# Optimization experiments

Hardware: AMD Instinct MI355X
Metric: run time of the kernel (lower is better)

## Reference

```python
import jax, jax.numpy as jnp
import numpy as np

N, n, D1, D2 = 16, 1024, 64, 64


def setup_inputs() -> dict:
    key = jax.random.key(0)
    ks = jax.random.split(key, 17)
    f = lambda k, shape: jax.random.normal(k, shape, dtype=jnp.float32)
    return {
        "A": f(ks[0], (N, n, n)),
        "X": f(ks[1], (N, n, D1)),
        "coeffs": f(ks[2], (5,)),
        "wA1": f(ks[3], (1, D1)),
        "wA2": f(ks[4], (1, D1)),
        "w11": f(ks[5], (D2, D1)),
        "w12": f(ks[6], (D2, D1)),
        "w13": f(ks[7], (D2, 1)),
        "w14": f(ks[8], (D2, 1)),
        "w15": f(ks[9], (D2, 1)),
        "w16": f(ks[10], (D2, 1)),
        "w21": f(ks[11], (D2, D1)),
        "w22": f(ks[12], (D2, D1)),
        "w23": f(ks[13], (D2, 1)),
        "w24": f(ks[14], (D2, 1)),
        "w25": f(ks[15], (D2, 1)),
        "w26": f(ks[16], (D2, 1)),
    }


def reference(A, X, coeffs, wA1, wA2, w11, w12, w13, w14, w15, w16,
              w21, w22, w23, w24, w25, w26):
    nn_ = A.shape[-1]
    diag = jnp.diagonal(A, axis1=-2, axis2=-1)          # (N, n)
    mean_diag = diag.mean(-1)                            # (N,)
    rowmean = A.mean(-1)                                 # (N, n) mean over columns
    mean_all = rowmean.mean(-1)                          # (N,)
    mean_X = X.mean(1)                                   # (N, D1)

    p1 = X @ wA1[0]                                      # (N, n)   Linear(D1->1) per node
    p2 = mean_X @ wA2[0]                                 # (N,)     Linear(D1->1) on mean

    # adjacency transform: scalar-weighted A + scalar stats + symmetrized row stats
    A_t = (coeffs[0] * A
           + (coeffs[1] * mean_all + coeffs[2] * mean_diag + p2)[:, None, None]
           + coeffs[3] * (rowmean[:, None, :] + rowmean[:, :, None])
           + coeffs[4] * (diag[:, None, :] + diag[:, :, None])
           + p1[:, None, :] + p1[:, :, None])             # (N, n, n)

    def node_transform(w_x, w_mx, w_col, w_diag, w_mdiag, w_mall):
        per_graph = (mean_X @ w_mx.T                      # (N, D2)
                     + mean_diag[:, None] * w_mdiag[:, 0][None, :]
                     + mean_all[:, None] * w_mall[:, 0][None, :])
        return (jnp.einsum('bnd,ed->bne', X, w_x)         # (N, n, D2)
                + rowmean[:, :, None] * w_col[:, 0]
                + diag[:, :, None] * w_diag[:, 0]
                + per_graph[:, None, :])

    X1_t = node_transform(w11, w12, w13, w14, w15, w16)
    X2_t = node_transform(w21, w22, w23, w24, w25, w26)

    out = A_t @ X2_t / nn_ + X1_t                         # (N, n, D2)
    return (A_t, out)
```

## Files before the change

### kernel.cpp

```cpp
#include <hip/hip_runtime.h>
#include <hip/hip_bf16.h>

#define NGRAPH 16
#define NNODE 1024
#define DDIM 64

typedef __attribute__((ext_vector_type(8))) short bf16x8;
typedef __attribute__((ext_vector_type(4))) float f32x4;

#define OFF_ROWSUM 0
#define OFF_DIAG   16384
#define OFF_P1     32768
#define OFF_R      49152
#define OFF_CS     65536
#define OFF_S      73728
#define OFF_S2P    75840
#define OFF_R2P    92224
#define OFF_BASE0  110656
#define OFF_X2T    1159232

__device__ __forceinline__ unsigned short f2bf(float f) {
    unsigned int u = __float_as_uint(f);
    u = (u + 0x7fffu + ((u >> 16) & 1u)) >> 16;
    return (unsigned short)u;
}

__device__ __forceinline__ float wave_reduce(float v) {
    #pragma unroll
    for (int off = 32; off; off >>= 1) v += __shfl_down(v, off, 64);
    return v;
}

__global__ __launch_bounds__(256) void kA_stats(const float* __restrict__ A,
                                                const float* __restrict__ X,
                                                const float* __restrict__ wA1,
                                                float* __restrict__ rowsum,
                                                float* __restrict__ diagv,
                                                float* __restrict__ p1,
                                                float* __restrict__ colsum_part) {
    if (blockIdx.x < NGRAPH * NNODE / 4) {
        int row  = blockIdx.x * 4 + (threadIdx.x >> 6);
        int lane = threadIdx.x & 63;
        const float4* b4 = (const float4*)(A + (size_t)row * NNODE);
        float sum = 0.f;
        #pragma unroll
        for (int it = 0; it < 4; ++it) {
            float4 v = b4[lane + it * 64];
            sum += v.x + v.y + v.z + v.w;
        }
        sum = wave_reduce(sum);
        if (lane == 0) {
            rowsum[row] = sum;
            int i = row & (NNODE - 1);
            diagv[row] = ((const float*)b4)[i];
        }
    } else {
        int bid  = blockIdx.x - NGRAPH * NNODE / 4;
        int b    = bid >> 3;
        int blk  = bid & 7;
        int wv   = threadIdx.x >> 6;
        int lane = threadIdx.x & 63;
        float w = wA1[lane];
        float cs = 0.f;
        int row0 = blk * 128 + wv * 32;
        const float* Xb = X + (size_t)b * NNODE * DDIM;
        for (int rI = 0; rI < 32; ++rI) {
            int i = row0 + rI;
            float x = Xb[i * DDIM + lane];
            cs += x;
            float v = wave_reduce(x * w);
            if (lane == 0) p1[b * NNODE + i] = v;
        }
        __shared__ float csl[4][64];
        csl[wv][lane] = cs;
        __syncthreads();
        if (threadIdx.x < 64) {
            float t = csl[0][lane] + csl[1][lane] + csl[2][lane] + csl[3][lane];
            colsum_part[(b * 8 + blk) * 64 + lane] = t;
        }
    }
}

__global__ __launch_bounds__(256) void kB_nodes(const float* __restrict__ X,
                                                const float* __restrict__ coeffs,
                                                const float* __restrict__ wA2,
                                                const float* __restrict__ w11,
                                                const float* __restrict__ w12,
                                                const float* __restrict__ w13,
                                                const float* __restrict__ w14,
                                                const float* __restrict__ w15,
                                                const float* __restrict__ w16,
                                                const float* __restrict__ w21,
                                                const float* __restrict__ w22,
                                                const float* __restrict__ w23,
                                                const float* __restrict__ w24,
                                                const float* __restrict__ w25,
                                                const float* __restrict__ w26,
                                                const float* __restrict__ rowsum,
                                                const float* __restrict__ diagv,
                                                const float* __restrict__ colsum_part,
                                                const float* __restrict__ p1g,
                                                float* __restrict__ rws,
                                                float* __restrict__ base0,
                                                unsigned short* __restrict__ x2tg,
                                                float* __restrict__ S2part,
                                                float* __restrict__ R2part,
                                                float* __restrict__ sArr) {
    __shared__ float Xl[64][68];
    __shared__ float w1l[64][68];
    __shared__ float w2l[64][68];
    __shared__ unsigned short X2Tl[64][68];
    __shared__ float rm_l[64], dg_l[64], r_l[64];
    __shared__ float redS[4][64], redR[4][64];
    __shared__ float redA[4], redD[4];
    __shared__ float mxs[64], p2s;
    __shared__ float pg1_l[64], pg2_l[64];

    int b    = blockIdx.x >> 4;
    int tile = blockIdx.x & 15;
    int i0   = tile * 64;
    int tid  = threadIdx.x;
    int e    = tid & 63;
    int wv   = tid >> 6;

    const float* Xg = X + (size_t)b * (NNODE * DDIM) + (size_t)i0 * DDIM;
    #pragma unroll
    for (int it = 0; it < 4; ++it) {
        int g   = it * 256 + tid;
        int row = g >> 4;
        int c4  = (g & 15) << 2;
        float4 v  = ((const float4*)Xg)[g];
        *(float4*)&Xl[row][c4] = v;
        float4 v1 = ((const float4*)w11)[g];
        *(float4*)&w1l[row][c4] = v1;
        float4 v2 = ((const float4*)w21)[g];
        *(float4*)&w2l[row][c4] = v2;
    }

    float sa = 0.f, sd = 0.f;
    for (int i = tid; i < NNODE; i += 256) {
        sa += rowsum[b * NNODE + i];
        sd += diagv[b * NNODE + i];
    }
    sa = wave_reduce(sa); sd = wave_reduce(sd);
    if (e == 0) { redA[wv] = sa; redD[wv] = sd; }
    if (tid < 64) {
        float mx = 0.f;
        for (int k = 0; k < 8; ++k) mx += colsum_part[(b * 8 + k) * 64 + tid];
        mxs[tid] = mx * (1.f / (float)NNODE);
    }
    __syncthreads();
    float mean_all  = (redA[0] + redA[1] + redA[2] + redA[3]) * (1.f / ((float)NNODE * (float)NNODE));
    float mean_diag = (redD[0] + redD[1] + redD[2] + redD[3]) * (1.f / (float)NNODE);
    if (tid < 64) {
        float v = wave_reduce(mxs[tid] * wA2[tid]);
        if (tid == 0) p2s = v;
    }
    if (tid < 64) {
        float a1 = 0.f, a2 = 0.f;
        for (int d = 0; d < 64; ++d) {
            float m = mxs[d];
            a1 += m * w12[tid * 64 + d];
            a2 += m * w22[tid * 64 + d];
        }
        pg1_l[tid] = a1 + mean_diag * w15[tid] + mean_all * w16[tid];
        pg2_l[tid] = a2 + mean_diag * w25[tid] + mean_all * w26[tid];
    }
    float c3 = coeffs[3], c4c = coeffs[4];
    if (tid < 64) {
        float rs  = rowsum[b * NNODE + i0 + tid];
        float dgv = diagv[b * NNODE + i0 + tid];
        float rmv = rs * (1.f / (float)NNODE);
        rm_l[tid] = rmv;
        dg_l[tid] = dgv;
        float rv = c3 * rmv + c4c * dgv + p1g[b * NNODE + i0 + tid];
        r_l[tid] = rv;
        rws[b * NNODE + i0 + tid] = rv;
    }
    __syncthreads();
    if (tile == 0 && tid == 0)
        sArr[b] = coeffs[1] * mean_all + coeffs[2] * mean_diag + p2s;

    float w13e = w13[e], w14e = w14[e], w23e = w23[e], w24e = w24[e];
    float pg1e = pg1_l[e], pg2e = pg2_l[e];

    float acc1[16], acc2[16];
    #pragma unroll
    for (int t = 0; t < 16; ++t) { acc1[t] = 0.f; acc2[t] = 0.f; }

    for (int d0 = 0; d0 < 64; d0 += 4) {
        float4 w1v = *(const float4*)&w1l[e][d0];
        float4 w2v = *(const float4*)&w2l[e][d0];
        #pragma unroll
        for (int t = 0; t < 16; ++t) {
            int li = wv + 4 * t;
            float4 xv = *(const float4*)&Xl[li][d0];
            acc1[t] += xv.x * w1v.x + xv.y * w1v.y + xv.z * w1v.z + xv.w * w1v.w;
            acc2[t] += xv.x * w2v.x + xv.y * w2v.y + xv.z * w2v.z + xv.w * w2v.w;
        }
    }

    float s2acc = 0.f, r2acc = 0.f;
    #pragma unroll
    for (int t = 0; t < 16; ++t) {
        int li = wv + 4 * t;
        int i  = i0 + li;
        float rmv = rm_l[li], dgv = dg_l[li];
        float x2t = acc2[t] + rmv * w23e + dgv * w24e + pg2e;
        float b0  = acc1[t] + rmv * w13e + dgv * w14e + pg1e;
        base0[((size_t)(b * NNODE + i)) * 64 + e] = b0;
        X2Tl[e][li] = f2bf(x2t);
        s2acc += x2t;
        r2acc += r_l[li] * x2t;
    }
    redS[wv][e] = s2acc;
    redR[wv][e] = r2acc;
    __syncthreads();

    for (int k = 0; k < 16; ++k) {
        int ep = wv * 16 + k;
        unsigned short v = X2Tl[ep][e];
        x2tg[((size_t)(b * 64 + ep)) * NNODE + i0 + e] = v;
    }
    if (tid < 64) {
        float s2 = redS[0][tid] + redS[1][tid] + redS[2][tid] + redS[3][tid];
        float r2 = redR[0][tid] + redR[1][tid] + redR[2][tid] + redR[3][tid];
        S2part[(b * 16 + tile) * 64 + tid] = s2;
        R2part[(b * 16 + tile) * 64 + tid] = r2;
    }
}

__global__ __launch_bounds__(512) void kC_main(const float* __restrict__ A,
                                               const float* __restrict__ coeffs,
                                               const float* __restrict__ sArr,
                                               const float* __restrict__ rArr,
                                               const unsigned short* __restrict__ x2tg,
                                               const float* __restrict__ base0,
                                               const float* __restrict__ S2part,
                                               const float* __restrict__ R2part,
                                               float* __restrict__ At,
                                               float* __restrict__ outp) {
    __shared__ unsigned short Al[32][136];
    __shared__ unsigned short X2l[64][136];
    __shared__ float r_lds[1024];
    __shared__ float s2_lds[64], r2_lds[64];

    int b    = blockIdx.x >> 5;
    int tile = blockIdx.x & 31;
    int i0   = tile * 32;
    int tid  = threadIdx.x;

    if (tid < 256) {
        float4 rv = ((const float4*)(rArr + b * NNODE))[tid];
        *(float4*)&r_lds[tid * 4] = rv;
    } else if (tid < 320) {
        int e = tid - 256;
        float s2 = 0.f, r2 = 0.f;
        #pragma unroll
        for (int t = 0; t < 16; ++t) {
            s2 += S2part[(b * 16 + t) * 64 + e];
            r2 += R2part[(b * 16 + t) * 64 + e];
        }
        s2_lds[e] = s2 * (1.f / (float)NNODE);
        r2_lds[e] = r2 * (1.f / (float)NNODE);
    }

    float sb  = sArr[b];
    float c0  = coeffs[0];
    float c0n = c0 * (1.f / (float)NNODE);

    int arow = tid >> 4;
    int acol = (tid & 15) * 8;
    const float* Ab  = A  + ((size_t)(b * NNODE + i0 + arow)) * NNODE + acol;
    float*       Atb = At + ((size_t)(b * NNODE + i0 + arow)) * NNODE + acol;
    int xe = tid >> 3;
    int xc = (tid & 7) * 16;
    const unsigned short* X2g = x2tg + ((size_t)(b * 64 + xe)) * NNODE + xc;

    int lane = tid & 63, wv = tid >> 6;
    int m = lane & 15, quad = lane >> 4;
    int rh = wv >> 2;
    int e0 = (wv & 3) * 16;

    f32x4 acc = {0.f, 0.f, 0.f, 0.f};

    for (int kt = 0; kt < 8; ++kt) {
        __syncthreads();

        float4 a0 = *(const float4*)(Ab + kt * 128);
        float4 a1 = *(const float4*)(Ab + kt * 128 + 4);
        float  ri = r_lds[i0 + arow];
        int cidx = kt * 128 + acol;
        float4 rj0 = *(const float4*)&r_lds[cidx];
        float4 rj1 = *(const float4*)&r_lds[cidx + 4];
        float bse = sb + ri;
        f32x4 t0, t1;
        t0.x = c0 * a0.x + bse + rj0.x; t0.y = c0 * a0.y + bse + rj0.y;
        t0.z = c0 * a0.z + bse + rj0.z; t0.w = c0 * a0.w + bse + rj0.w;
        t1.x = c0 * a1.x + bse + rj1.x; t1.y = c0 * a1.y + bse + rj1.y;
        t1.z = c0 * a1.z + bse + rj1.z; t1.w = c0 * a1.w + bse + rj1.w;
        __builtin_nontemporal_store(t0, (f32x4*)(Atb + kt * 128));
        __builtin_nontemporal_store(t1, (f32x4*)(Atb + kt * 128 + 4));

        unsigned int p0 = (unsigned int)f2bf(a0.x) | ((unsigned int)f2bf(a0.y) << 16);
        unsigned int p1 = (unsigned int)f2bf(a0.z) | ((unsigned int)f2bf(a0.w) << 16);
        unsigned int p2 = (unsigned int)f2bf(a1.x) | ((unsigned int)f2bf(a1.y) << 16);
        unsigned int p3 = (unsigned int)f2bf(a1.z) | ((unsigned int)f2bf(a1.w) << 16);
        uint4 pk = {p0, p1, p2, p3};
        *(uint4*)&Al[arow][acol] = pk;

        uint4 xv0 = *(const uint4*)(X2g + (size_t)kt * 128);
        uint4 xv1 = *(const uint4*)(X2g + (size_t)kt * 128 + 8);
        *(uint4*)&X2l[xe][xc]     = xv0;
        *(uint4*)&X2l[xe][xc + 8] = xv1;
        __syncthreads();

        #pragma unroll
        for (int ks = 0; ks < 4; ++ks) {
            int k0 = ks * 32 + quad * 8;
            bf16x8 av = *(const bf16x8*)&Al[rh * 16 + m][k0];
            bf16x8 bv = *(const bf16x8*)&X2l[e0 + m][k0];
            acc = __builtin_amdgcn_mfma_f32_16x16x32_bf16(av, bv, acc, 0, 0, 0);
        }
    }

    int e = e0 + m;
    float s2 = s2_lds[e];
    float r2 = r2_lds[e];
    #pragma unroll
    for (int reg = 0; reg < 4; ++reg) {
        int i = i0 + rh * 16 + quad * 4 + reg;
        float v = acc[reg] * c0n
                + base0[((size_t)(b * NNODE + i)) * 64 + e]
                + (sb + r_lds[i]) * s2 + r2;
        outp[((size_t)(b * NNODE + i)) * 64 + e] = v;
    }
}

extern "C" void kernel_launch(void* const* d_in, const int* in_sizes, int n_in,
                              void* d_out, int out_size, void* d_ws, size_t ws_size,
                              hipStream_t stream) {
    const float* A      = (const float*)d_in[0];
    const float* X      = (const float*)d_in[1];
    const float* coeffs = (const float*)d_in[2];
    const float* wA1    = (const float*)d_in[3];
    const float* wA2    = (const float*)d_in[4];
    const float* w11    = (const float*)d_in[5];
    const float* w12    = (const float*)d_in[6];
    const float* w13    = (const float*)d_in[7];
    const float* w14    = (const float*)d_in[8];
    const float* w15    = (const float*)d_in[9];
    const float* w16    = (const float*)d_in[10];
    const float* w21    = (const float*)d_in[11];
    const float* w22    = (const float*)d_in[12];
    const float* w23    = (const float*)d_in[13];
    const float* w24    = (const float*)d_in[14];
    const float* w25    = (const float*)d_in[15];
    const float* w26    = (const float*)d_in[16];

    float* ws  = (float*)d_ws;
    float* At  = (float*)d_out;
    float* out = (float*)d_out + (size_t)NGRAPH * NNODE * NNODE;

    float* rowsum = ws + OFF_ROWSUM;
    float* diagv  = ws + OFF_DIAG;
    float* p1     = ws + OFF_P1;
    float* rws    = ws + OFF_R;
    float* cspart = ws + OFF_CS;
    float* sArr   = ws + OFF_S;
    float* S2part = ws + OFF_S2P;
    float* R2part = ws + OFF_R2P;
    float* base0  = ws + OFF_BASE0;
    unsigned short* x2tg = (unsigned short*)(ws + OFF_X2T);

    kA_stats<<<NGRAPH * NNODE / 4 + NGRAPH * 8, 256, 0, stream>>>(
        A, X, wA1, rowsum, diagv, p1, cspart);
    kB_nodes<<<NGRAPH * 16, 256, 0, stream>>>(
        X, coeffs, wA2, w11, w12, w13, w14, w15, w16,
        w21, w22, w23, w24, w25, w26,
        rowsum, diagv, cspart, p1,
        rws, base0, x2tg, S2part, R2part, sArr);
    kC_main<<<NGRAPH * 32, 512, 0, stream>>>(
        A, coeffs, sArr, rws, x2tg, base0, S2part, R2part, At, out);
}
```

Baseline: 217.8 us.

## Shrink main kernel tiles to 16 rows, load X2 operand straight from global

The main fused kernel now processes 16 rows per block with 256 threads and 1024 blocks instead of 32 rows with 512 threads. The X2 operand is loaded directly from global memory into MFMA registers rather than staged through shared memory, and the A tile uses a double-buffered LDS slot so each step needs only one barrier. The A_t stores also switch from nontemporal to ordinary stores. This cuts LDS traffic and barriers and adds parallelism, but each block now rereads the whole X2 slice, so global and L2 reads of X2 roughly double.

New measurement: 204.3 us. 1.07x faster.

```diff
diff --git a/kernel.cpp b/kernel.cpp
--- a/kernel.cpp
+++ b/kernel.cpp
@@ -230,7 +230,7 @@
     }
 }
 
-__global__ __launch_bounds__(512) void kC_main(const float* __restrict__ A,
+__global__ __launch_bounds__(256) void kC_main(const float* __restrict__ A,
                                                const float* __restrict__ coeffs,
                                                const float* __restrict__ sArr,
                                                const float* __restrict__ rArr,
@@ -240,29 +240,26 @@
                                                const float* __restrict__ R2part,
                                                float* __restrict__ At,
                                                float* __restrict__ outp) {
-    __shared__ unsigned short Al[32][136];
-    __shared__ unsigned short X2l[64][136];
+    __shared__ unsigned short Al[2][16][136];
     __shared__ float r_lds[1024];
     __shared__ float s2_lds[64], r2_lds[64];
 
-    int b    = blockIdx.x >> 5;
-    int tile = blockIdx.x & 31;
-    int i0   = tile * 32;
+    int b    = blockIdx.x >> 6;
+    int tile = blockIdx.x & 63;
+    int i0   = tile * 16;
     int tid  = threadIdx.x;
 
-    if (tid < 256) {
-        float4 rv = ((const float4*)(rArr + b * NNODE))[tid];
-        *(float4*)&r_lds[tid * 4] = rv;
-    } else if (tid < 320) {
-        int e = tid - 256;
+    float4 rv = ((const float4*)(rArr + b * NNODE))[tid];
+    *(float4*)&r_lds[tid * 4] = rv;
+    if (tid < 64) {
         float s2 = 0.f, r2 = 0.f;
         #pragma unroll
         for (int t = 0; t < 16; ++t) {
-            s2 += S2part[(b * 16 + t) * 64 + e];
-            r2 += R2part[(b * 16 + t) * 64 + e];
-        }
-        s2_lds[e] = s2 * (1.f / (float)NNODE);
-        r2_lds[e] = r2 * (1.f / (float)NNODE);
+            s2 += S2part[(b * 16 + t) * 64 + tid];
+            r2 += R2part[(b * 16 + t) * 64 + tid];
+        }
+        s2_lds[tid] = s2 * (1.f / (float)NNODE);
+        r2_lds[tid] = r2 * (1.f / (float)NNODE);
     }
 
     float sb  = sArr[b];
@@ -273,19 +270,21 @@
     int acol = (tid & 15) * 8;
     const float* Ab  = A  + ((size_t)(b * NNODE + i0 + arow)) * NNODE + acol;
     float*       Atb = At + ((size_t)(b * NNODE + i0 + arow)) * NNODE + acol;
-    int xe = tid >> 3;
-    int xc = (tid & 7) * 16;
-    const unsigned short* X2g = x2tg + ((size_t)(b * 64 + xe)) * NNODE + xc;
 
     int lane = tid & 63, wv = tid >> 6;
     int m = lane & 15, quad = lane >> 4;
-    int rh = wv >> 2;
-    int e0 = (wv & 3) * 16;
+    int e = wv * 16 + m;
+    const unsigned short* Bg = x2tg + ((size_t)(b * 64 + e)) * NNODE + quad * 8;
 
     f32x4 acc = {0.f, 0.f, 0.f, 0.f};
 
+    __syncthreads();
+
     for (int kt = 0; kt < 8; ++kt) {
-        __syncthreads();
+        bf16x8 bf0 = *(const bf16x8*)(Bg + kt * 128);
+        bf16x8 bf1 = *(const bf16x8*)(Bg + kt * 128 + 32);
+        bf16x8 bf2 = *(const bf16x8*)(Bg + kt * 128 + 64);
+        bf16x8 bf3 = *(const bf16x8*)(Bg + kt * 128 + 96);
 
         float4 a0 = *(const float4*)(Ab + kt * 128);
         float4 a1 = *(const float4*)(Ab + kt * 128 + 4);
@@ -294,42 +293,38 @@
         float4 rj0 = *(const float4*)&r_lds[cidx];
         float4 rj1 = *(const float4*)&r_lds[cidx + 4];
         float bse = sb + ri;
-        f32x4 t0, t1;
+        float4 t0, t1;
         t0.x = c0 * a0.x + bse + rj0.x; t0.y = c0 * a0.y + bse + rj0.y;
         t0.z = c0 * a0.z + bse + rj0.z; t0.w = c0 * a0.w + bse + rj0.w;
         t1.x = c0 * a1.x + bse + rj1.x; t1.y = c0 * a1.y + bse + rj1.y;
         t1.z = c0 * a1.z + bse + rj1.z; t1.w = c0 * a1.w + bse + rj1.w;
-        __builtin_nontemporal_store(t0, (f32x4*)(Atb + kt * 128));
-        __builtin_nontemporal_store(t1, (f32x4*)(Atb + kt * 128 + 4));
+        *(float4*)(Atb + kt * 128)     = t0;
+        *(float4*)(Atb + kt * 128 + 4) = t1;
 
         unsigned int p0 = (unsigned int)f2bf(a0.x) | ((unsigned int)f2bf(a0.y) << 16);
         unsigned int p1 = (unsigned int)f2bf(a0.z) | ((unsigned int)f2bf(a0.w) << 16);
         unsigned int p2 = (unsigned int)f2bf(a1.x) | ((unsigned int)f2bf(a1.y) << 16);
         unsigned int p3 = (unsigned int)f2bf(a1.z) | ((unsigned int)f2bf(a1.w) << 16);
         uint4 pk = {p0, p1, p2, p3};
-        *(uint4*)&Al[arow][acol] = pk;
-
-        uint4 xv0 = *(const uint4*)(X2g + (size_t)kt * 128);
-        uint4 xv1 = *(const uint4*)(X2g + (size_t)kt * 128 + 8);
-        *(uint4*)&X2l[xe][xc]     = xv0;
-        *(uint4*)&X2l[xe][xc + 8] = xv1;
+        *(uint4*)&Al[kt & 1][arow][acol] = pk;
+
         __syncthreads();
 
-        #pragma unroll
-        for (int ks = 0; ks < 4; ++ks) {
-            int k0 = ks * 32 + quad * 8;
-            bf16x8 av = *(const bf16x8*)&Al[rh * 16 + m][k0];
-            bf16x8 bv = *(const bf16x8*)&X2l[e0 + m][k0];
-            acc = __builtin_amdgcn_mfma_f32_16x16x32_bf16(av, bv, acc, 0, 0, 0);
-        }
-    }
-
-    int e = e0 + m;
+        bf16x8 av0 = *(const bf16x8*)&Al[kt & 1][m][quad * 8];
+        bf16x8 av1 = *(const bf16x8*)&Al[kt & 1][m][32 + quad * 8];
+        bf16x8 av2 = *(const bf16x8*)&Al[kt & 1][m][64 + quad * 8];
+        bf16x8 av3 = *(const bf16x8*)&Al[kt & 1][m][96 + quad * 8];
+        acc = __builtin_amdgcn_mfma_f32_16x16x32_bf16(av0, bf0, acc, 0, 0, 0);
+        acc = __builtin_amdgcn_mfma_f32_16x16x32_bf16(av1, bf1, acc, 0, 0, 0);
+        acc = __builtin_amdgcn_mfma_f32_16x16x32_bf16(av2, bf2, acc, 0, 0, 0);
+        acc = __builtin_amdgcn_mfma_f32_16x16x32_bf16(av3, bf3, acc, 0, 0, 0);
+    }
+
     float s2 = s2_lds[e];
     float r2 = r2_lds[e];
     #pragma unroll
     for (int reg = 0; reg < 4; ++reg) {
-        int i = i0 + rh * 16 + quad * 4 + reg;
+        int i = i0 + quad * 4 + reg;
         float v = acc[reg] * c0n
                 + base0[((size_t)(b * NNODE + i)) * 64 + e]
                 + (sb + r_lds[i]) * s2 + r2;
@@ -380,6 +375,6 @@
         w21, w22, w23, w24, w25, w26,
         rowsum, diagv, cspart, p1,
         rws, base0, x2tg, S2part, R2part, sArr);
-    kC_main<<<NGRAPH * 32, 512, 0, stream>>>(
+    kC_main<<<NGRAPH * 64, 256, 0, stream>>>(
         A, coeffs, sArr, rws, x2tg, base0, S2part, R2part, At, out);
 }
```
